# Kernel optimization log

Hardware: AMD Instinct MI355X
Metric: run time of the kernel (lower is better)

Reference implementation:

```python
import jax, jax.numpy as jnp
import numpy as np
from jax import lax


def setup_inputs() -> dict:
    key = jax.random.key(0)
    ks = jax.random.split(key, 16)
    f32 = jnp.float32
    g = lambda k, shp, s=0.02: jax.random.normal(k, shp, dtype=f32) * s
    inp = {
        "x": jax.random.normal(ks[0], (4, 1, 4096), dtype=f32),
        # conv_time: Conv1d(1,128,3,pad=1)
        "conv_time_w": g(ks[1], (128, 1, 3)), "conv_time_b": jnp.zeros((128,), f32),
        "bn0_g": jnp.ones((128,), f32), "bn0_b": jnp.zeros((128,), f32),
        "bn0_m": jnp.zeros((128,), f32), "bn0_v": jnp.ones((128,), f32),
        # block1: Conv1d(128,256,3,pad=1)+BN
        "conv1_w": g(ks[2], (256, 128, 3)), "conv1_b": jnp.zeros((256,), f32),
        "bn1_g": jnp.ones((256,), f32), "bn1_b": jnp.zeros((256,), f32),
        "bn1_m": jnp.zeros((256,), f32), "bn1_v": jnp.ones((256,), f32),
        # block2: Conv1d(256,512,3,pad=1)+BN
        "conv2_w": g(ks[3], (512, 256, 3)), "conv2_b": jnp.zeros((512,), f32),
        "bn2_g": jnp.ones((512,), f32), "bn2_b": jnp.zeros((512,), f32),
        "bn2_m": jnp.zeros((512,), f32), "bn2_v": jnp.ones((512,), f32),
        # GAT 1: fc Linear(512,512), attn_fc Linear(1024,1)
        "gat1_fc_w": g(ks[4], (512, 512)), "gat1_fc_b": jnp.zeros((512,), f32),
        "gat1_attn_w": g(ks[5], (1024,)), "gat1_attn_b": jnp.zeros((), f32),
        # GAT 2: fc Linear(512,256), attn_fc Linear(512,1)
        "gat2_fc_w": g(ks[6], (256, 512)), "gat2_fc_b": jnp.zeros((256,), f32),
        "gat2_attn_w": g(ks[7], (512,)), "gat2_attn_b": jnp.zeros((), f32),
        # head: Linear(256,2)
        "fc_w": g(ks[8], (2, 256)), "fc_b": jnp.zeros((2,), f32),
    }
    return inp


def _conv1d(x, w, b):
    # x: [B,C,T], w: [O,C,3], padding=1
    y = lax.conv_general_dilated(x, w, window_strides=(1,), padding=((1, 1),),
                                 dimension_numbers=("NCH", "OIH", "NCH"))
    return y + b[None, :, None]


def _bn(x, g, b, m, v):
    # eval-mode BatchNorm1d over channel dim
    return (x - m[None, :, None]) * (g * lax.rsqrt(v + 1e-5))[None, :, None] + b[None, :, None]


def _maxpool2(x):
    return lax.reduce_window(x, -jnp.inf, lax.max, (1, 1, 2), (1, 1, 2), "VALID")


def _gat(x2d, fc_w, fc_b, aw, ab):
    # Faithful to: cat([h_i, h_j]) @ attn_w == h_i @ aw[:d] + h_j @ aw[d:]
    h = x2d @ fc_w.T + fc_b           # [N, d]
    d = h.shape[-1]
    s1 = h @ aw[:d]                   # [N] (query part, h.repeat(1,N))
    s2 = h @ aw[d:]                   # [N] (key part,   h.repeat(N,1))
    e = jax.nn.leaky_relu(s1[:, None] + s2[None, :] + ab, negative_slope=0.01)  # [N,N]
    att = jax.nn.softmax(e, axis=1)
    return att @ h                    # [N, d]


def reference(x, conv_time_w, conv_time_b, bn0_g, bn0_b, bn0_m, bn0_v,
              conv1_w, conv1_b, bn1_g, bn1_b, bn1_m, bn1_v,
              conv2_w, conv2_b, bn2_g, bn2_b, bn2_m, bn2_v,
              gat1_fc_w, gat1_fc_b, gat1_attn_w, gat1_attn_b,
              gat2_fc_w, gat2_fc_b, gat2_attn_w, gat2_attn_b,
              fc_w, fc_b):
    h = jax.nn.relu(_bn(_conv1d(x, conv_time_w, conv_time_b), bn0_g, bn0_b, bn0_m, bn0_v))
    h = _maxpool2(jax.nn.relu(_bn(_conv1d(h, conv1_w, conv1_b), bn1_g, bn1_b, bn1_m, bn1_v)))
    h = _maxpool2(jax.nn.relu(_bn(_conv1d(h, conv2_w, conv2_b), bn2_g, bn2_b, bn2_m, bn2_v)))
    h = jnp.transpose(h, (0, 2, 1))   # [B, S, 512]
    B, S, C = h.shape
    g = h.reshape(B * S, C)           # whole batch flattened into one graph (as in source)
    g = _gat(g, gat1_fc_w, gat1_fc_b, gat1_attn_w, gat1_attn_b)   # [N, 512]
    g = _gat(g, gat2_fc_w, gat2_fc_b, gat2_attn_w, gat2_attn_b)   # [N, 256]
    pooled = g.reshape(B, S, -1).mean(axis=1)                     # [B, 256]
    return pooled @ fc_w.T + fc_b     # [B, 2] (dropout is identity in eval)
```

## Files before the change

### kernel.cpp

```cpp
#include <hip/hip_runtime.h>
#include <hip/hip_bf16.h>
#include <math.h>


#define NN 4096
#define BB 4
#define TT0 4096

__global__ void k_conv_time2(const float* __restrict__ x, const float* __restrict__ w,
                             const float* __restrict__ cb, const float* __restrict__ g,
                             const float* __restrict__ bbp, const float* __restrict__ m,
                             const float* __restrict__ v, float* __restrict__ out) {
  int gid = blockIdx.x * 256 + threadIdx.x;
  int t4 = gid & 1023;
  int o = (gid >> 10) & 127;
  int b = gid >> 17;
  int t = t4 * 4;
  float sc = g[o] * rsqrtf(v[o] + 1e-5f);
  float sh = (cb[o] - m[o]) * sc + bbp[o];
  const float* xb = x + b * 4096;
  float4 xc = *(const float4*)&xb[t];
  float xm = (t > 0) ? xb[t - 1] : 0.f;
  float xp = (t + 4 < 4096) ? xb[t + 4] : 0.f;
  const float* wo = w + o * 3;
  float w0 = wo[0], w1 = wo[1], w2 = wo[2];
  float4 y;
  y.x = fmaxf((w0 * xm   + w1 * xc.x + w2 * xc.y) * sc + sh, 0.f);
  y.y = fmaxf((w0 * xc.x + w1 * xc.y + w2 * xc.z) * sc + sh, 0.f);
  y.z = fmaxf((w0 * xc.y + w1 * xc.z + w2 * xc.w) * sc + sh, 0.f);
  y.w = fmaxf((w0 * xc.z + w1 * xc.w + w2 * xp  ) * sc + sh, 0.f);
  *(float4*)&out[((size_t)(b * 128) + o) * 4096 + t] = y;
}

template <int C, int TIN>
__global__ __launch_bounds__(256, 4)
void k_conv_pool7(const float* __restrict__ in, const float* __restrict__ w,
                  const float* __restrict__ cb, const float* __restrict__ g,
                  const float* __restrict__ bbp, const float* __restrict__ m,
                  const float* __restrict__ v, float* __restrict__ out, int OCH) {
  constexpr int TOUT = TIN / 2;
  constexpr int CC = 32;
  __shared__ float xs[CC][264];

  int bx = blockIdx.x;
  int nT = TIN / 256;
  int tb = bx % nT;
  int ob = (bx / nT) % (OCH / 16);
  int b  = bx / (nT * (OCH / 16));
  int tid = threadIdx.x;
  int lane = tid & 63;
  int wv = __builtin_amdgcn_readfirstlane(tid >> 6);
  int t0 = tb * 256;

  float acc[4][4];
  #pragma unroll
  for (int i = 0; i < 4; i++)
    #pragma unroll
    for (int p = 0; p < 4; p++) acc[i][p] = 0.f;

  const float* wq = w + (size_t)(ob * 16 + wv * 4) * C * 3;

  for (int c0 = 0; c0 < C; c0 += CC) {
    for (int u = 0; u < 9; u++) {
      int e4 = tid + 256 * u;
      if (e4 < CC * 66) {
        int cc = e4 / 66, j4 = e4 - cc * 66;
        int t = t0 - 4 + 4 * j4;
        const float* src = &in[((size_t)(b * C) + c0 + cc) * TIN + t];
        float4 val;
        if (t >= 0 && t + 3 < TIN) {
          val = *(const float4*)src;
        } else {
          val.x = (t     >= 0 && t     < TIN) ? src[0] : 0.f;
          val.y = (t + 1 >= 0 && t + 1 < TIN) ? src[1] : 0.f;
          val.z = (t + 2 >= 0 && t + 2 < TIN) ? src[2] : 0.f;
          val.w = (t + 3 >= 0 && t + 3 < TIN) ? src[3] : 0.f;
        }
        *(float4*)&xs[cc][4 * j4] = val;
      }
    }
    __syncthreads();
    #pragma unroll 4
    for (int cc = 0; cc < CC; ++cc) {
      float w0[4], w1[4], w2[4];
      #pragma unroll
      for (int oi = 0; oi < 4; oi++) {
        const float* wr = wq + ((size_t)oi * C + c0 + cc) * 3;
        w0[oi] = wr[0]; w1[oi] = wr[1]; w2[oi] = wr[2];
      }
      float2 xl = *(const float2*)&xs[cc][4 * lane + 2];
      float4 xc = *(const float4*)&xs[cc][4 * lane + 4];
      float2 xr = *(const float2*)&xs[cc][4 * lane + 8];
      float xv[6] = {xl.y, xc.x, xc.y, xc.z, xc.w, xr.x};
      #pragma unroll
      for (int oi = 0; oi < 4; oi++)
        #pragma unroll
        for (int p = 0; p < 4; p++)
          acc[oi][p] += w0[oi] * xv[p] + w1[oi] * xv[p + 1] + w2[oi] * xv[p + 2];
    }
    __syncthreads();
  }

  int base_o = ob * 16 + wv * 4;
  #pragma unroll
  for (int oi = 0; oi < 4; oi++) {
    int o = base_o + oi;
    float sc = g[o] * rsqrtf(v[o] + 1e-5f);
    float sh = (cb[o] - m[o]) * sc + bbp[o];
    float2 r;
    r.x = fmaxf(fmaxf(acc[oi][0] * sc + sh, acc[oi][1] * sc + sh), 0.f);
    r.y = fmaxf(fmaxf(acc[oi][2] * sc + sh, acc[oi][3] * sc + sh), 0.f);
    *(float2*)&out[((size_t)(b * OCH) + o) * TOUT + tb * 128 + 2 * lane] = r;
  }
}

__global__ __launch_bounds__(512, 1)
void k_gemm_chw(const float* __restrict__ A, const float* __restrict__ Wt,
                const float* __restrict__ bias, float* __restrict__ Cout) {
  constexpr int K = 512, N = 512;
  __shared__ float As[32][132];
  __shared__ float Bs[32][68];
  int i0 = blockIdx.x * 128, j0 = blockIdx.y * 64;
  int tid = threadIdx.x;
  int tx = tid & 15, ty = tid >> 4;
  int b = i0 >> 10, s0 = i0 & 1023;
  const float* Ab = A + (size_t)b * K * 1024 + s0;

  float acc[4][4];
  #pragma unroll
  for (int ii = 0; ii < 4; ii++)
    #pragma unroll
    for (int jj = 0; jj < 4; jj++) acc[ii][jj] = 0.f;

  int ka = (tid + 0) >> 5, i4a = tid & 31;
  int kb = (tid + 512) >> 5, i4b = tid & 31;
  float4 pa0, pa1; float pb[4];

  pa0 = *(const float4*)&Ab[(size_t)ka * 1024 + 4 * i4a];
  pa1 = *(const float4*)&Ab[(size_t)kb * 1024 + 4 * i4b];
  #pragma unroll
  for (int r = 0; r < 4; r++) {
    int e = tid + 512 * r; int j = e >> 5, k = e & 31;
    pb[r] = Wt[(size_t)(j0 + j) * K + k];
  }

  for (int kt = 0; kt < K; kt += 32) {
    *(float4*)&As[ka][4 * i4a] = pa0;
    *(float4*)&As[kb][4 * i4b] = pa1;
    #pragma unroll
    for (int r = 0; r < 4; r++) {
      int e = tid + 512 * r; int j = e >> 5, k = e & 31;
      Bs[k][j] = pb[r];
    }
    __syncthreads();
    int ktn = (kt + 32 < K) ? kt + 32 : 0;
    float4 na0 = *(const float4*)&Ab[(size_t)(ktn + ka) * 1024 + 4 * i4a];
    float4 na1 = *(const float4*)&Ab[(size_t)(ktn + kb) * 1024 + 4 * i4b];
    float nb[4];
    #pragma unroll
    for (int r = 0; r < 4; r++) {
      int e = tid + 512 * r; int j = e >> 5, k = e & 31;
      nb[r] = Wt[(size_t)(j0 + j) * K + ktn + k];
    }
    #pragma unroll 4
    for (int kk = 0; kk < 32; ++kk) {
      float4 a4 = *(const float4*)&As[kk][ty * 4];
      float4 b4 = *(const float4*)&Bs[kk][tx * 4];
      float a[4] = {a4.x, a4.y, a4.z, a4.w};
      float bv[4] = {b4.x, b4.y, b4.z, b4.w};
      #pragma unroll
      for (int ii = 0; ii < 4; ii++)
        #pragma unroll
        for (int jj = 0; jj < 4; jj++) acc[ii][jj] += a[ii] * bv[jj];
    }
    __syncthreads();
    pa0 = na0; pa1 = na1;
    #pragma unroll
    for (int r = 0; r < 4; r++) pb[r] = nb[r];
  }

  float4 bias4 = *(const float4*)&bias[j0 + 4 * tx];
  #pragma unroll
  for (int ii = 0; ii < 4; ii++) {
    int i = i0 + ty * 4 + ii;
    float4 o4;
    o4.x = acc[ii][0] + bias4.x; o4.y = acc[ii][1] + bias4.y;
    o4.z = acc[ii][2] + bias4.z; o4.w = acc[ii][3] + bias4.w;
    *(float4*)&Cout[(size_t)i * N + j0 + 4 * tx] = o4;
  }
}

__global__ __launch_bounds__(256, 2)
void k_gemm_rm(const float* __restrict__ A, const float* __restrict__ Wt,
               const float* __restrict__ bias, float* __restrict__ Cout) {
  constexpr int K = 512, N = 256;
  __shared__ float As[32][68];
  __shared__ float Bs[32][68];
  int i0 = blockIdx.x * 64, j0 = blockIdx.y * 64;
  int tid = threadIdx.x;
  int tx = tid & 15, ty = tid >> 4;

  float acc[4][4];
  #pragma unroll
  for (int ii = 0; ii < 4; ii++)
    #pragma unroll
    for (int jj = 0; jj < 4; jj++) acc[ii][jj] = 0.f;

  float4 pa[2]; float pb[8];
  #pragma unroll
  for (int r = 0; r < 2; r++) {
    int e4 = tid + 256 * r; int i = e4 >> 3, k4 = e4 & 7;
    pa[r] = *(const float4*)&A[(size_t)(i0 + i) * K + 4 * k4];
  }
  #pragma unroll
  for (int r = 0; r < 8; r++) {
    int e = tid + 256 * r; int j = e >> 5, k = e & 31;
    pb[r] = Wt[(size_t)(j0 + j) * K + k];
  }

  for (int kt = 0; kt < K; kt += 32) {
    #pragma unroll
    for (int r = 0; r < 2; r++) {
      int e4 = tid + 256 * r; int i = e4 >> 3, k4 = e4 & 7;
      As[4 * k4 + 0][i] = pa[r].x; As[4 * k4 + 1][i] = pa[r].y;
      As[4 * k4 + 2][i] = pa[r].z; As[4 * k4 + 3][i] = pa[r].w;
    }
    #pragma unroll
    for (int r = 0; r < 8; r++) {
      int e = tid + 256 * r; int j = e >> 5, k = e & 31;
      Bs[k][j] = pb[r];
    }
    __syncthreads();
    int ktn = (kt + 32 < K) ? kt + 32 : 0;
    float4 na[2]; float nb[8];
    #pragma unroll
    for (int r = 0; r < 2; r++) {
      int e4 = tid + 256 * r; int i = e4 >> 3, k4 = e4 & 7;
      na[r] = *(const float4*)&A[(size_t)(i0 + i) * K + ktn + 4 * k4];
    }
    #pragma unroll
    for (int r = 0; r < 8; r++) {
      int e = tid + 256 * r; int j = e >> 5, k = e & 31;
      nb[r] = Wt[(size_t)(j0 + j) * K + ktn + k];
    }
    #pragma unroll 4
    for (int kk = 0; kk < 32; ++kk) {
      float4 a4 = *(const float4*)&As[kk][ty * 4];
      float4 b4 = *(const float4*)&Bs[kk][tx * 4];
      float a[4] = {a4.x, a4.y, a4.z, a4.w};
      float bv[4] = {b4.x, b4.y, b4.z, b4.w};
      #pragma unroll
      for (int ii = 0; ii < 4; ii++)
        #pragma unroll
        for (int jj = 0; jj < 4; jj++) acc[ii][jj] += a[ii] * bv[jj];
    }
    __syncthreads();
    pa[0] = na[0]; pa[1] = na[1];
    #pragma unroll
    for (int r = 0; r < 8; r++) pb[r] = nb[r];
  }

  float4 bias4 = *(const float4*)&bias[j0 + 4 * tx];
  #pragma unroll
  for (int ii = 0; ii < 4; ii++) {
    int i = i0 + ty * 4 + ii;
    float4 o4;
    o4.x = acc[ii][0] + bias4.x; o4.y = acc[ii][1] + bias4.y;
    o4.z = acc[ii][2] + bias4.z; o4.w = acc[ii][3] + bias4.w;
    *(float4*)&Cout[(size_t)i * N + j0 + 4 * tx] = o4;
  }
}

template <int D>
__global__ void k_rowdot(const float* __restrict__ h, const float* __restrict__ aw,
                         float* __restrict__ s1, float* __restrict__ s2,
                         int* __restrict__ rnk) {
  if (blockIdx.x < 16) rnk[blockIdx.x * 256 + threadIdx.x] = 0;
  int wid = threadIdx.x >> 6, lane = threadIdx.x & 63;
  int i = blockIdx.x * 4 + wid;
  const float* hr = h + (size_t)i * D;
  float d1 = 0.f, d2 = 0.f;
  #pragma unroll
  for (int d = lane; d < D; d += 64) {
    float hv = hr[d];
    d1 += hv * aw[d];
    d2 += hv * aw[D + d];
  }
  for (int off = 32; off; off >>= 1) {
    d1 += __shfl_down(d1, off, 64);
    d2 += __shfl_down(d2, off, 64);
  }
  if (lane == 0) { s1[i] = d1; s2[i] = d2; }
}

__global__ void k_rank(const float* __restrict__ s2v, int* __restrict__ rnk) {
  __shared__ float ls[1024];
  int j = blockIdx.x * 256 + threadIdx.x;
  int base = blockIdx.y * 1024;
  float vj = s2v[j];
  for (int e = threadIdx.x; e < 1024; e += 256) ls[e] = s2v[base + e];
  __syncthreads();
  int cnt = 0;
  #pragma unroll 8
  for (int r = 0; r < 1024; ++r) {
    float vr = ls[r];
    cnt += (vr < vj || (vr == vj && (base + r) < j)) ? 1 : 0;
  }
  atomicAdd(&rnk[j], cnt);
}

__global__ void k_scatter(const float* __restrict__ s2v, const int* __restrict__ rnk,
                          float* __restrict__ svals, int* __restrict__ sidx) {
  int j = blockIdx.x * 256 + threadIdx.x;
  int r = rnk[j];
  svals[r] = s2v[j];
  sidx[r] = j;
}

__global__ void k_tw(const float* __restrict__ s1, const float* __restrict__ svals,
                     const float* __restrict__ abp, int* __restrict__ tarr,
                     float* __restrict__ Aarr, float* __restrict__ Barr,
                     float* __restrict__ wp, float* __restrict__ wm) {
  int i = blockIdx.x * 256 + threadIdx.x;
  float ab = abp[0], M2 = svals[NN - 1];
  float alpha = s1[i] + ab;
  float cthr = -alpha;
  int lo = 0, hi = NN;
  while (lo < hi) {
    int mid = (lo + hi) >> 1;
    if (svals[mid] < cthr) lo = mid + 1; else hi = mid;
  }
  tarr[i] = lo;
  float e1 = alpha + M2;
  float gam = fmaxf(e1, 0.01f * e1);
  Aarr[i] = expf(e1 - gam);
  Barr[i] = expf(0.01f * e1 - gam);
  float d = svals[i] - M2;
  wp[i] = expf(d);
  wm[i] = expf(0.01f * d);
}

__global__ void k_scan_den(const float* __restrict__ wp, const float* __restrict__ wm,
                           float* __restrict__ preden, float* __restrict__ sufden) {
  __shared__ float csP[256], csM[256];
  int tid = threadIdx.x;
  int base = tid * 16;
  float sm = 0.f, sp = 0.f;
  for (int u = 0; u < 16; u++) { sm += wm[base + u]; sp += wp[base + u]; }
  csM[tid] = sm; csP[tid] = sp;
  __syncthreads();
  float offM = 0.f;
  for (int c = 0; c < tid; c++) offM += csM[c];
  float offP = 0.f;
  for (int c = tid + 1; c < 256; c++) offP += csP[c];
  float run = offM;
  for (int u = 0; u < 16; u++) { preden[base + u] = run; run += wm[base + u]; }
  if (tid == 255) preden[NN] = run;
  float runp = offP;
  if (tid == 255) sufden[NN] = 0.f;
  for (int u = 15; u >= 0; u--) { runp += wp[base + u]; sufden[base + u] = runp; }
}

template <int D>
__global__ void k_chunksum(const float* __restrict__ h, const int* __restrict__ sidx,
                           const float* __restrict__ wp, const float* __restrict__ wm,
                           float* __restrict__ csP, float* __restrict__ csM) {
  constexpr int CPT = D / 256;
  int c = blockIdx.x, tid = threadIdx.x;
  __shared__ int lidx[32];
  __shared__ float lwp[32], lwm[32];
  if (tid < 32) {
    int r = c * 32 + tid;
    lidx[tid] = sidx[r]; lwp[tid] = wp[r]; lwm[tid] = wm[r];
  }
  __syncthreads();
  float aP[CPT], aM[CPT];
  #pragma unroll
  for (int q = 0; q < CPT; q++) { aP[q] = 0.f; aM[q] = 0.f; }
  for (int u = 0; u < 32; u++) {
    const float* hr = h + (size_t)lidx[u] * D;
    float fp = lwp[u], fm = lwm[u];
    #pragma unroll
    for (int q = 0; q < CPT; q++) {
      float hv = hr[tid + q * 256];
      aP[q] += fp * hv; aM[q] += fm * hv;
    }
  }
  #pragma unroll
  for (int q = 0; q < CPT; q++) {
    csP[(size_t)c * D + tid + q * 256] = aP[q];
    csM[(size_t)c * D + tid + q * 256] = aM[q];
  }
}

template <int D>
__global__ void k_chunkoff(const float* __restrict__ csP, const float* __restrict__ csM,
                           float* __restrict__ offP, float* __restrict__ offM) {
  int d = blockIdx.x * 256 + threadIdx.x;
  float rm = 0.f;
  for (int cb = 0; cb < 128; cb += 16) {
    float vals[16];
    #pragma unroll
    for (int u = 0; u < 16; u++) vals[u] = csM[(size_t)(cb + u) * D + d];
    #pragma unroll
    for (int u = 0; u < 16; u++) { offM[(size_t)(cb + u) * D + d] = rm; rm += vals[u]; }
  }
  float rp = 0.f;
  for (int cb = 127; cb >= 15; cb -= 16) {
    float vals[16];
    #pragma unroll
    for (int u = 0; u < 16; u++) vals[u] = csP[(size_t)(cb - u) * D + d];
    #pragma unroll
    for (int u = 0; u < 16; u++) { offP[(size_t)(cb - u) * D + d] = rp; rp += vals[u]; }
  }
}

template <int D>
__global__ void k_scanwrite(const float* __restrict__ h, const int* __restrict__ sidx,
                            const float* __restrict__ wp, const float* __restrict__ wm,
                            const float* __restrict__ offP, const float* __restrict__ offM,
                            float* __restrict__ Pre, float* __restrict__ Suf) {
  constexpr int CPT = D / 256;
  int c = blockIdx.x, tid = threadIdx.x;
  __shared__ int lidx[32];
  __shared__ float lwp[32], lwm[32];
  if (tid < 32) {
    int r = c * 32 + tid;
    lidx[tid] = sidx[r]; lwp[tid] = wp[r]; lwm[tid] = wm[r];
  }
  __syncthreads();
  float runM[CPT], runP[CPT];
  #pragma unroll
  for (int q = 0; q < CPT; q++) {
    int d = tid + q * 256;
    runM[q] = offM[(size_t)c * D + d];
    runP[q] = offP[(size_t)c * D + d];
  }
  for (int u = 0; u < 32; u++) {
    const float* hr = h + (size_t)lidx[u] * D;
    float fm = lwm[u];
    #pragma unroll
    for (int q = 0; q < CPT; q++) {
      int d = tid + q * 256;
      Pre[(size_t)(c * 32 + u) * D + d] = runM[q];
      runM[q] += fm * hr[d];
    }
  }
  if (c == 127) {
    #pragma unroll
    for (int q = 0; q < CPT; q++) Pre[(size_t)NN * D + tid + q * 256] = runM[q];
    #pragma unroll
    for (int q = 0; q < CPT; q++) Suf[(size_t)NN * D + tid + q * 256] = 0.f;
  }
  for (int u = 31; u >= 0; u--) {
    const float* hr = h + (size_t)lidx[u] * D;
    float fp = lwp[u];
    #pragma unroll
    for (int q = 0; q < CPT; q++) {
      int d = tid + q * 256;
      runP[q] += fp * hr[d];
      Suf[(size_t)(c * 32 + u) * D + d] = runP[q];
    }
  }
}

template <int D>
__global__ void k_apply(const float* __restrict__ Pre, const float* __restrict__ Suf,
                        const float* __restrict__ preden, const float* __restrict__ sufden,
                        const int* __restrict__ tarr, const float* __restrict__ Aarr,
                        const float* __restrict__ Barr, float* __restrict__ outg) {
  int i = blockIdx.x;
  int t = tarr[i];
  float A = Aarr[i], Bv = Barr[i];
  float den = A * sufden[t] + Bv * preden[t];
  float inv = 1.f / den;
  const float* Pr = Pre + (size_t)t * D;
  const float* Sr = Suf + (size_t)t * D;
  for (int d = threadIdx.x; d < D; d += 256)
    outg[(size_t)i * D + d] = (A * Sr[d] + Bv * Pr[d]) * inv;
}

__global__ void k_pool(const float* __restrict__ g2, float* __restrict__ pp) {
  int b = blockIdx.x >> 4, ch = blockIdx.x & 15;
  const float* base = g2 + ((size_t)(b * 1024) + ch * 64) * 256 + threadIdx.x;
  float s = 0.f;
  for (int r = 0; r < 64; r++) s += base[(size_t)r * 256];
  pp[(size_t)blockIdx.x * 256 + threadIdx.x] = s;
}

__global__ void k_head2(const float* __restrict__ pp, const float* __restrict__ fcw,
                        const float* __restrict__ fcb, float* __restrict__ out) {
  __shared__ float pooled[4][256];
  int tid = threadIdx.x;
  for (int b = 0; b < 4; b++) {
    float s = 0.f;
    for (int ch = 0; ch < 16; ch++) s += pp[(size_t)(b * 16 + ch) * 256 + tid];
    pooled[b][tid] = s * (1.f / 1024.f);
  }
  __syncthreads();
  if (tid < 8) {
    int b = tid >> 1, c = tid & 1;
    float acc = fcb[c];
    for (int cc = 0; cc < 256; cc++) acc += pooled[b][cc] * fcw[c * 256 + cc];
    out[b * 2 + c] = acc;
  }
}

extern "C" void kernel_launch(void* const* d_in, const int* in_sizes, int n_in,
                              void* d_out, int out_size, void* d_ws, size_t ws_size,
                              hipStream_t stream) {
  const float* x    = (const float*)d_in[0];
  const float* ctw  = (const float*)d_in[1];
  const float* ctb  = (const float*)d_in[2];
  const float* bn0g = (const float*)d_in[3];
  const float* bn0b = (const float*)d_in[4];
  const float* bn0m = (const float*)d_in[5];
  const float* bn0v = (const float*)d_in[6];
  const float* c1w  = (const float*)d_in[7];
  const float* c1b  = (const float*)d_in[8];
  const float* bn1g = (const float*)d_in[9];
  const float* bn1b = (const float*)d_in[10];
  const float* bn1m = (const float*)d_in[11];
  const float* bn1v = (const float*)d_in[12];
  const float* c2w  = (const float*)d_in[13];
  const float* c2b  = (const float*)d_in[14];
  const float* bn2g = (const float*)d_in[15];
  const float* bn2b = (const float*)d_in[16];
  const float* bn2m = (const float*)d_in[17];
  const float* bn2v = (const float*)d_in[18];
  const float* g1w  = (const float*)d_in[19];
  const float* g1b  = (const float*)d_in[20];
  const float* g1aw = (const float*)d_in[21];
  const float* g1ab = (const float*)d_in[22];
  const float* g2w  = (const float*)d_in[23];
  const float* g2b  = (const float*)d_in[24];
  const float* g2aw = (const float*)d_in[25];
  const float* g2ab = (const float*)d_in[26];
  const float* fcw  = (const float*)d_in[27];
  const float* fcb  = (const float*)d_in[28];
  float* ws = (float*)d_ws;

  const size_t SLOT = (size_t)(NN + 1) * 512;
  float* slot0 = ws;
  float* slot1 = ws + SLOT;
  float* slot2 = ws + 2 * SLOT;
  float* slot3 = ws + 3 * SLOT;
  float* sm    = ws + 4 * SLOT;
  float* s1    = sm;
  float* s2    = sm + 4096;
  float* svals = sm + 8192;
  int*   sidx  = (int*)(sm + 12288);
  int*   tarr  = (int*)(sm + 16384);
  float* Aarr  = sm + 20480;
  float* Barr  = sm + 24576;
  float* wp    = sm + 28672;
  float* wm    = sm + 32768;
  float* preden = sm + 36864;
  float* sufden = sm + 40968;
  float* csP   = sm + 45072;
  float* csM   = csP + 65536;
  float* offP  = csM + 65536;
  float* offM  = offP + 65536;
  int*   rnk   = (int*)(offM + 65536);
  float* pp    = offM + 65536 + 4096;

  k_conv_time2<<<BB * 128 * 1024 / 256, 256, 0, stream>>>(x, ctw, ctb, bn0g, bn0b, bn0m, bn0v, slot0);
  k_conv_pool7<128, 4096><<<BB * 16 * 16, 256, 0, stream>>>(
      slot0, c1w, c1b, bn1g, bn1b, bn1m, bn1v, slot1, 256);
  k_conv_pool7<256, 2048><<<BB * 32 * 8, 256, 0, stream>>>(
      slot1, c2w, c2b, bn2g, bn2b, bn2m, bn2v, slot2, 512);

  k_gemm_chw<<<dim3(32, 8), 512, 0, stream>>>(slot2, g1w, g1b, slot3);
  k_rowdot<512><<<NN / 4, 256, 0, stream>>>(slot3, g1aw, s1, s2, rnk);
  k_rank<<<dim3(16, 4), 256, 0, stream>>>(s2, rnk);
  k_scatter<<<16, 256, 0, stream>>>(s2, rnk, svals, sidx);
  k_tw<<<NN / 256, 256, 0, stream>>>(s1, svals, g1ab, tarr, Aarr, Barr, wp, wm);
  k_scan_den<<<1, 256, 0, stream>>>(wp, wm, preden, sufden);
  k_chunksum<512><<<128, 256, 0, stream>>>(slot3, sidx, wp, wm, csP, csM);
  k_chunkoff<512><<<2, 256, 0, stream>>>(csP, csM, offP, offM);
  k_scanwrite<512><<<128, 256, 0, stream>>>(slot3, sidx, wp, wm, offP, offM, slot1, slot0);
  k_apply<512><<<NN, 256, 0, stream>>>(slot1, slot0, preden, sufden, tarr, Aarr, Barr, slot2);

  k_gemm_rm<<<dim3(64, 4), 256, 0, stream>>>(slot2, g2w, g2b, slot3);
  k_rowdot<256><<<NN / 4, 256, 0, stream>>>(slot3, g2aw, s1, s2, rnk);
  k_rank<<<dim3(16, 4), 256, 0, stream>>>(s2, rnk);
  k_scatter<<<16, 256, 0, stream>>>(s2, rnk, svals, sidx);
  k_tw<<<NN / 256, 256, 0, stream>>>(s1, svals, g2ab, tarr, Aarr, Barr, wp, wm);
  k_scan_den<<<1, 256, 0, stream>>>(wp, wm, preden, sufden);
  k_chunksum<256><<<128, 256, 0, stream>>>(slot3, sidx, wp, wm, csP, csM);
  k_chunkoff<256><<<1, 256, 0, stream>>>(csP, csM, offP, offM);
  k_scanwrite<256><<<128, 256, 0, stream>>>(slot3, sidx, wp, wm, offP, offM, slot1, slot0);
  k_apply<256><<<NN, 256, 0, stream>>>(slot1, slot0, preden, sufden, tarr, Aarr, Barr, slot2);

  k_pool<<<BB * 16, 256, 0, stream>>>(slot2, pp);
  k_head2<<<1, 256, 0, stream>>>(pp, fcw, fcb, (float*)d_out);
}
```

Measured before the change: 403.6 us.

## Widen conv-pool tile to 8 output channels per wave with shuffle-based halo exchange

The conv+BN+ReLU+maxpool kernel now gives each wave 8 output channels instead of 4, so each block covers 32 channels and the grid is halved. Per input channel, a thread reads only its own float4 from shared memory. The neighbour-tap contributions are kept as separate partial sums and exchanged across lanes with shuffles in the epilogue, with tile-edge values read directly from LDS. This cuts LDS traffic and reuses each loaded x value across more channels, at the cost of more accumulator registers, fewer blocks for occupancy, and uniform weight loads that now cover 8 channels.

Result: slower. 453.6 us (+12.4%).

```diff
diff --git a/kernel.cpp b/kernel.cpp
--- a/kernel.cpp
+++ b/kernel.cpp
@@ -34,7 +34,7 @@
 
 template <int C, int TIN>
 __global__ __launch_bounds__(256, 4)
-void k_conv_pool7(const float* __restrict__ in, const float* __restrict__ w,
+void k_conv_pool8(const float* __restrict__ in, const float* __restrict__ w,
                   const float* __restrict__ cb, const float* __restrict__ g,
                   const float* __restrict__ bbp, const float* __restrict__ m,
                   const float* __restrict__ v, float* __restrict__ out, int OCH) {
@@ -45,22 +45,24 @@
   int bx = blockIdx.x;
   int nT = TIN / 256;
   int tb = bx % nT;
-  int ob = (bx / nT) % (OCH / 16);
-  int b  = bx / (nT * (OCH / 16));
+  int ob = (bx / nT) % (OCH / 32);
+  int b  = bx / (nT * (OCH / 32));
   int tid = threadIdx.x;
   int lane = tid & 63;
   int wv = __builtin_amdgcn_readfirstlane(tid >> 6);
   int t0 = tb * 256;
 
-  float acc[4][4];
-  #pragma unroll
-  for (int i = 0; i < 4; i++)
-    #pragma unroll
-    for (int p = 0; p < 4; p++) acc[i][p] = 0.f;
-
-  const float* wq = w + (size_t)(ob * 16 + wv * 4) * C * 3;
+  float A1[8], A2[8], A3[8], A4[8], E[8], F[8], GE[8], GF[8];
+  #pragma unroll
+  for (int oi = 0; oi < 8; oi++) {
+    A1[oi] = A2[oi] = A3[oi] = A4[oi] = 0.f;
+    E[oi] = F[oi] = GE[oi] = GF[oi] = 0.f;
+  }
+
+  const float* wq = w + (size_t)(ob * 32 + wv * 8) * C * 3;
 
   for (int c0 = 0; c0 < C; c0 += CC) {
+    #pragma unroll
     for (int u = 0; u < 9; u++) {
       int e4 = tid + 256 * u;
       if (e4 < CC * 66) {
@@ -80,36 +82,43 @@
       }
     }
     __syncthreads();
-    #pragma unroll 4
+    #pragma unroll 2
     for (int cc = 0; cc < CC; ++cc) {
-      float w0[4], w1[4], w2[4];
+      float4 X = *(const float4*)&xs[cc][4 * lane + 4];
+      float xb3   = xs[cc][3];
+      float xb260 = xs[cc][260];
       #pragma unroll
-      for (int oi = 0; oi < 4; oi++) {
+      for (int oi = 0; oi < 8; oi++) {
         const float* wr = wq + ((size_t)oi * C + c0 + cc) * 3;
-        w0[oi] = wr[0]; w1[oi] = wr[1]; w2[oi] = wr[2];
+        float w0 = wr[0], w1 = wr[1], w2 = wr[2];
+        A1[oi] += w1 * X.x + w2 * X.y;
+        A2[oi] += w0 * X.x + w1 * X.y + w2 * X.z;
+        A3[oi] += w0 * X.y + w1 * X.z + w2 * X.w;
+        A4[oi] += w0 * X.z + w1 * X.w;
+        E[oi]  += w0 * X.w;
+        F[oi]  += w2 * X.x;
+        GE[oi] += w0 * xb3;
+        GF[oi] += w2 * xb260;
       }
-      float2 xl = *(const float2*)&xs[cc][4 * lane + 2];
-      float4 xc = *(const float4*)&xs[cc][4 * lane + 4];
-      float2 xr = *(const float2*)&xs[cc][4 * lane + 8];
-      float xv[6] = {xl.y, xc.x, xc.y, xc.z, xc.w, xr.x};
-      #pragma unroll
-      for (int oi = 0; oi < 4; oi++)
-        #pragma unroll
-        for (int p = 0; p < 4; p++)
-          acc[oi][p] += w0[oi] * xv[p] + w1[oi] * xv[p + 1] + w2[oi] * xv[p + 2];
     }
     __syncthreads();
   }
 
-  int base_o = ob * 16 + wv * 4;
-  #pragma unroll
-  for (int oi = 0; oi < 4; oi++) {
+  int base_o = ob * 32 + wv * 8;
+  #pragma unroll
+  for (int oi = 0; oi < 8; oi++) {
     int o = base_o + oi;
     float sc = g[o] * rsqrtf(v[o] + 1e-5f);
     float sh = (cb[o] - m[o]) * sc + bbp[o];
-    float2 r;
-    r.x = fmaxf(fmaxf(acc[oi][0] * sc + sh, acc[oi][1] * sc + sh), 0.f);
-    r.y = fmaxf(fmaxf(acc[oi][2] * sc + sh, acc[oi][3] * sc + sh), 0.f);
+    float eIn = __shfl_up(E[oi], 1, 64);
+    if (lane == 0) eIn = GE[oi];
+    float fIn = __shfl_down(F[oi], 1, 64);
+    if (lane == 63) fIn = GF[oi];
+    float y0 = A1[oi] + eIn;
+    float y3 = A4[oi] + fIn;
+    float p0 = fmaxf(fmaxf(y0 * sc + sh, A2[oi] * sc + sh), 0.f);
+    float p1 = fmaxf(fmaxf(A3[oi] * sc + sh, y3 * sc + sh), 0.f);
+    float2 r; r.x = p0; r.y = p1;
     *(float2*)&out[((size_t)(b * OCH) + o) * TOUT + tb * 128 + 2 * lane] = r;
   }
 }
@@ -565,9 +574,9 @@
   float* pp    = offM + 65536 + 4096;
 
   k_conv_time2<<<BB * 128 * 1024 / 256, 256, 0, stream>>>(x, ctw, ctb, bn0g, bn0b, bn0m, bn0v, slot0);
-  k_conv_pool7<128, 4096><<<BB * 16 * 16, 256, 0, stream>>>(
+  k_conv_pool8<128, 4096><<<BB * 8 * 16, 256, 0, stream>>>(
       slot0, c1w, c1b, bn1g, bn1b, bn1m, bn1v, slot1, 256);
-  k_conv_pool7<256, 2048><<<BB * 32 * 8, 256, 0, stream>>>(
+  k_conv_pool8<256, 2048><<<BB * 16 * 8, 256, 0, stream>>>(
       slot1, c2w, c2b, bn2g, bn2b, bn2m, bn2v, slot2, 512);
 
   k_gemm_chw<<<dim3(32, 8), 512, 0, stream>>>(slot2, g1w, g1b, slot3);
```
